# Performance work log

Measured on AMD Instinct MI355X. Metric: run time of the kernel, lower is better.

The kernel has to match this reference:

```python
import jax, jax.numpy as jnp
import numpy as np

HIDDEN = 1024
N_HEAD = 16
HEAD_DIM = HIDDEN // N_HEAD

def setup_inputs() -> dict:
    key = jax.random.key(0)
    ks = jax.random.split(key, 5)
    B, T = 2, 2048
    s_in = 1.0 / np.sqrt(HIDDEN)
    return {
        "x": jax.random.normal(ks[0], (B, T, HIDDEN), dtype=jnp.float32),
        "w_attn": jax.random.normal(ks[1], (HIDDEN, 3 * HIDDEN), dtype=jnp.float32) * s_in,
        "b_attn": jnp.zeros((3 * HIDDEN,), dtype=jnp.float32),
        "w_proj": jax.random.normal(ks[2], (HIDDEN, HIDDEN), dtype=jnp.float32) * s_in,
        "b_proj": jnp.zeros((HIDDEN,), dtype=jnp.float32),
    }

def reference(x, w_attn, b_attn, w_proj, b_proj):
    B, T, C = x.shape
    qkv = x @ w_attn + b_attn  # (B, T, 3C)
    q, k, v = jnp.split(qkv, 3, axis=-1)
    # (B, H, T, D)
    q = q.reshape(B, T, N_HEAD, HEAD_DIM).transpose(0, 2, 1, 3)
    k = k.reshape(B, T, N_HEAD, HEAD_DIM).transpose(0, 2, 1, 3)
    v = v.reshape(B, T, N_HEAD, HEAD_DIM).transpose(0, 2, 1, 3)
    scale = 1.0 / np.sqrt(HEAD_DIM).astype(np.float32)
    attn = jnp.einsum('bhqd,bhkd->bhqk', q, k) * scale
    causal = jnp.tril(jnp.ones((T, T), dtype=bool))
    attn = jnp.where(causal[None, None], attn, -jnp.inf)
    attn = jax.nn.softmax(attn, axis=-1)
    out = jnp.einsum('bhqk,bhkd->bhqd', attn, v)
    out = out.transpose(0, 2, 1, 3).reshape(B, T, C)
    return out @ w_proj + b_proj
```

## Files before the change

### kernel.cpp

```cpp
#include <hip/hip_runtime.h>
#include <stdint.h>

#define T_SEQ 2048
#define NB 2
#define NH 16
#define HD 64
#define HID 1024
#define MTOK (NB * T_SEQ)

typedef float f32x4 __attribute__((ext_vector_type(4)));
typedef float f32x16 __attribute__((ext_vector_type(16)));
typedef short bf16x8 __attribute__((ext_vector_type(8)));
typedef unsigned short u16;
typedef unsigned int u32;

#define QSCALE 0.1803368801f

__device__ __forceinline__ u16 f2bf(float f) {
  union { float f; uint32_t u; } v; v.f = f;
  return (u16)((v.u + 0x7fffu + ((v.u >> 16) & 1u)) >> 16);
}

__device__ __forceinline__ void gl_lds16(const void* g, void* l) {
  __builtin_amdgcn_global_load_lds(
      (const __attribute__((address_space(1))) unsigned int*)g,
      (__attribute__((address_space(3))) unsigned int*)l, 16, 0, 0);
}

__global__ void convert_k(const float* __restrict__ in, u16* __restrict__ out, int n4) {
  int i = blockIdx.x * blockDim.x + threadIdx.x;
  int stride = gridDim.x * blockDim.x;
  for (; i < n4; i += stride) {
    float4 f = ((const float4*)in)[i];
    ushort4 o;
    o.x = f2bf(f.x); o.y = f2bf(f.y); o.z = f2bf(f.z); o.w = f2bf(f.w);
    ((ushort4*)out)[i] = o;
  }
}

__global__ void transpose_k(const float* __restrict__ in, u16* __restrict__ out, int R, int C) {
  __shared__ float tile[32][33];
  int c0 = blockIdx.x * 32, r0 = blockIdx.y * 32;
  int tx = threadIdx.x, ty = threadIdx.y;
#pragma unroll
  for (int i = 0; i < 32; i += 8)
    tile[ty + i][tx] = in[(size_t)(r0 + ty + i) * C + c0 + tx];
  __syncthreads();
#pragma unroll
  for (int i = 0; i < 32; i += 8)
    out[(size_t)(c0 + ty + i) * R + r0 + tx] = f2bf(tile[tx][ty + i]);
}

template <int MODE>
__global__ __launch_bounds__(256, 4)
void gemm_k(const u16* __restrict__ A, const u16* __restrict__ Bt,
            const float* __restrict__ bias,
            u16* __restrict__ q, u16* __restrict__ kk, u16* __restrict__ v,
            float* __restrict__ outf) {
  __shared__ __align__(16) char lds[32768];
  const int tid = threadIdx.x, wid = tid >> 6, lane = tid & 63;
  const int m0 = blockIdx.y * 128, n0 = blockIdx.x * 128;
  const int wm = (wid >> 1) * 64, wn = (wid & 1) * 64;

  f32x4 acc[4][4];
  const f32x4 z = {0.f, 0.f, 0.f, 0.f};
#pragma unroll
  for (int mi = 0; mi < 4; ++mi)
#pragma unroll
    for (int ni = 0; ni < 4; ++ni) acc[mi][ni] = z;

  const int srow = tid >> 2;
  const int scb = (tid & 3) << 4;
  const int scsrc = (scb ^ ((srow & 3) << 4)) >> 1;
  const int rA = lane & 15;
  const int kbyte = (lane >> 4) << 4;

#define GSTAGE(tt_)                                                              \
  do {                                                                           \
    const int k0_ = (tt_) << 5;                                                  \
    char* ab_ = lds + (((tt_) & 1) << 13);                                       \
    char* bb_ = lds + 16384 + (((tt_) & 1) << 13);                               \
    gl_lds16(A + (size_t)(m0 + srow) * HID + k0_ + scsrc, ab_ + wid * 1024);     \
    gl_lds16(A + (size_t)(m0 + 64 + srow) * HID + k0_ + scsrc, ab_ + 4096 + wid * 1024); \
    gl_lds16(Bt + (size_t)(n0 + srow) * HID + k0_ + scsrc, bb_ + wid * 1024);    \
    gl_lds16(Bt + (size_t)(n0 + 64 + srow) * HID + k0_ + scsrc, bb_ + 4096 + wid * 1024); \
  } while (0)

  GSTAGE(0);
  GSTAGE(1);

  for (int tt = 0; tt < 32; ++tt) {
    if (tt < 31)
      asm volatile("s_waitcnt vmcnt(4)" ::: "memory");
    else
      asm volatile("s_waitcnt vmcnt(0)" ::: "memory");
    __builtin_amdgcn_s_barrier();
    __builtin_amdgcn_sched_barrier(0);

    const char* ab = lds + ((tt & 1) << 13);
    const char* bb = lds + 16384 + ((tt & 1) << 13);
    bf16x8 a[4], b[4];
#pragma unroll
    for (int mi = 0; mi < 4; ++mi) {
      const int row = wm + mi * 16 + rA;
      a[mi] = *(const bf16x8*)(ab + row * 64 + (kbyte ^ ((row & 3) << 4)));
    }
#pragma unroll
    for (int ni = 0; ni < 4; ++ni) {
      const int row = wn + ni * 16 + rA;
      b[ni] = *(const bf16x8*)(bb + row * 64 + (kbyte ^ ((row & 3) << 4)));
    }
#pragma unroll
    for (int mi = 0; mi < 4; ++mi)
#pragma unroll
      for (int ni = 0; ni < 4; ++ni)
        acc[mi][ni] = __builtin_amdgcn_mfma_f32_16x16x32_bf16(a[mi], b[ni], acc[mi][ni], 0, 0, 0);

    __builtin_amdgcn_s_barrier();
    __builtin_amdgcn_sched_barrier(0);
    if (tt < 30) GSTAGE(tt + 2);
  }
#undef GSTAGE

  const int coll = lane & 15, rowl = (lane >> 4) << 2;
#pragma unroll
  for (int mi = 0; mi < 4; ++mi) {
#pragma unroll
    for (int ni = 0; ni < 4; ++ni) {
      const int n = n0 + wn + ni * 16 + coll;
      const float bv = bias[n];
#pragma unroll
      for (int r = 0; r < 4; ++r) {
        const int m = m0 + wm + mi * 16 + rowl + r;
        float val = acc[mi][ni][r] + bv;
        if (MODE == 0) {
          const int reg = n >> 10, c = n & 1023, h = c >> 6, d = c & 63;
          const int bb2 = m >> 11, t = m & 2047;
          if (reg == 0) q[((size_t)(bb2 * NH + h) * T_SEQ + t) * HD + d] = f2bf(val * QSCALE);
          else if (reg == 1) kk[((size_t)(bb2 * NH + h) * T_SEQ + t) * HD + d] = f2bf(val);
          else v[((size_t)(bb2 * NH + h) * HD + d) * T_SEQ + t] = f2bf(val);
        } else {
          outf[(size_t)m * HID + n] = val;
        }
      }
    }
  }
}

__global__ __launch_bounds__(512, 4)
void attn_k(const u16* __restrict__ Q, const u16* __restrict__ K,
            const u16* __restrict__ Vt, u16* __restrict__ AO) {
  __shared__ __align__(16) char lds[65536];
  const int tid = threadIdx.x;
  const int lane = tid & 63;
  const int wid = tid >> 6;
  const int qsub = wid & 3, par = wid >> 2;
  const int bid = blockIdx.x;
  const int halfg = bid >> 8, r8 = bid & 255;
  const int bh = (r8 & 7) * 4 + ((r8 >> 3) & 3);
  const int lvl = r8 >> 5;
  const int qb = halfg ? lvl : (15 - lvl);
  const int q0 = qb * 128;
  const int ql = lane & 31, h = lane >> 5;
  const bool hi = (h != 0);

  const u16* Qg = Q + (size_t)bh * T_SEQ * HD;
  const u16* Kg = K + (size_t)bh * T_SEQ * HD;
  const u16* Vg = Vt + (size_t)bh * T_SEQ * HD;

  const int q0w = q0 + qsub * 32;
  const int dq = 2 * qb + (qsub >> 1);

  bf16x8 qf[4];
#pragma unroll
  for (int s = 0; s < 4; ++s)
    qf[s] = *(const bf16x8*)(Qg + (size_t)(q0w + ql) * HD + s * 16 + h * 8);

  f32x16 ot0, ot1;
#pragma unroll
  for (int i = 0; i < 16; ++i) { ot0[i] = 0.f; ot1[i] = 0.f; }
  float m = -3.0e38f, l = 0.f;

  const int srow = tid >> 3;
  const int scb = (tid & 7) << 4;
  const int sc0 = (scb ^ ((srow & 7) << 4)) >> 1;

  const int nsup = qb + 1;

#define STAGE(tt_)                                                            \
  do {                                                                        \
    const int kv0_ = (tt_) << 6;                                              \
    gl_lds16(Kg + (size_t)(kv0_ + srow) * HD + sc0,                           \
             lds + (((tt_) & 3) << 13) + wid * 1024);                         \
    gl_lds16(Vg + (size_t)srow * T_SEQ + kv0_ + sc0,                          \
             lds + 32768 + (((tt_) & 3) << 13) + wid * 1024);                 \
  } while (0)

  STAGE(0);
  STAGE(1);

  for (int ss = 0; ss < nsup; ++ss) {
    if (ss + 1 < nsup) {
      STAGE(2 * ss + 2);
      STAGE(2 * ss + 3);
      asm volatile("s_waitcnt vmcnt(4)" ::: "memory");
    } else {
      asm volatile("s_waitcnt vmcnt(0)" ::: "memory");
    }
    __builtin_amdgcn_s_barrier();
    __builtin_amdgcn_sched_barrier(0);

    const int tt = 2 * ss + par;
    if (tt <= dq) {
      const int kv0 = tt << 6;
      const char* kb = lds + ((tt & 3) << 13);
      const char* vb = lds + 32768 + ((tt & 3) << 13);
      f32x16 s0, s1;
#pragma unroll
      for (int i = 0; i < 16; ++i) { s0[i] = 0.f; s1[i] = 0.f; }
#pragma unroll
      for (int s = 0; s < 4; ++s) {
        const int cb = 32 * s + 16 * h;
        const int r0 = ql, r1 = 32 + ql;
        bf16x8 kf0 = *(const bf16x8*)(kb + r0 * 128 + (cb ^ ((r0 & 7) << 4)));
        bf16x8 kf1 = *(const bf16x8*)(kb + r1 * 128 + (cb ^ ((r1 & 7) << 4)));
        s0 = __builtin_amdgcn_mfma_f32_32x32x16_bf16(kf0, qf[s], s0, 0, 0, 0);
        s1 = __builtin_amdgcn_mfma_f32_32x32x16_bf16(kf1, qf[s], s1, 0, 0, 0);
      }
      if (tt == dq) {
        const int qg = q0w + ql;
#pragma unroll
        for (int r = 0; r < 16; ++r) {
          const int kvl = (r & 3) + 8 * (r >> 2) + 4 * h;
          if (kv0 + kvl > qg) s0[r] = -3.0e38f;
          if (kv0 + 32 + kvl > qg) s1[r] = -3.0e38f;
        }
      }
      float mx[16];
#pragma unroll
      for (int i = 0; i < 16; ++i) mx[i] = fmaxf(s0[i], s1[i]);
#pragma unroll
      for (int d = 8; d; d >>= 1)
#pragma unroll
        for (int i = 0; i < d; ++i) mx[i] = fmaxf(mx[i], mx[i + d]);
      const float tm = fmaxf(mx[0], __shfl_xor(mx[0], 32, 64));
      if (!__all(tm <= m + 4.0f)) {
        const float mnew = fmaxf(m, tm);
        const float fold = __builtin_amdgcn_exp2f(m - mnew);
        m = mnew;
        l *= fold;
#pragma unroll
        for (int i = 0; i < 16; ++i) { ot0[i] *= fold; ot1[i] *= fold; }
      }
#pragma unroll
      for (int i = 0; i < 16; ++i) {
        s0[i] = __builtin_amdgcn_exp2f(s0[i] - m);
        s1[i] = __builtin_amdgcn_exp2f(s1[i] - m);
      }
      float sm[16];
#pragma unroll
      for (int i = 0; i < 16; ++i) sm[i] = s0[i] + s1[i];
#pragma unroll
      for (int d = 8; d; d >>= 1)
#pragma unroll
        for (int i = 0; i < d; ++i) sm[i] += sm[i + d];
      l += sm[0] + __shfl_xor(sm[0], 32, 64);

      u32 w0[8], w1[8];
#pragma unroll
      for (int mm = 0; mm < 8; ++mm) {
        asm("v_cvt_pk_bf16_f32 %0, %1, %2" : "=v"(w0[mm]) : "v"(s0[2 * mm]), "v"(s0[2 * mm + 1]));
        asm("v_cvt_pk_bf16_f32 %0, %1, %2" : "=v"(w1[mm]) : "v"(s1[2 * mm]), "v"(s1[2 * mm + 1]));
      }
#pragma unroll
      for (int sb = 0; sb < 2; ++sb) {
#pragma unroll
        for (int t = 0; t < 2; ++t) {
          u32 a0 = sb ? w1[4 * t]     : w0[4 * t];
          u32 a1 = sb ? w1[4 * t + 1] : w0[4 * t + 1];
          u32 a2 = sb ? w1[4 * t + 2] : w0[4 * t + 2];
          u32 a3 = sb ? w1[4 * t + 3] : w0[4 * t + 3];
          u32 snd0 = hi ? a0 : a2;
          u32 snd1 = hi ? a1 : a3;
          u32 own0 = hi ? a2 : a0;
          u32 own1 = hi ? a3 : a1;
          u32 p0 = __shfl_xor(snd0, 32, 64);
          u32 p1 = __shfl_xor(snd1, 32, 64);
          union { u32 u[4]; bf16x8 v; } fr;
          fr.u[0] = hi ? p0 : own0;
          fr.u[1] = hi ? p1 : own1;
          fr.u[2] = hi ? own0 : p0;
          fr.u[3] = hi ? own1 : p1;
          const int s = sb * 2 + t;
          const int cb = 32 * s + 16 * h;
          const int r0 = ql, r1 = 32 + ql;
          bf16x8 vf0 = *(const bf16x8*)(vb + r0 * 128 + (cb ^ ((r0 & 7) << 4)));
          bf16x8 vf1 = *(const bf16x8*)(vb + r1 * 128 + (cb ^ ((r1 & 7) << 4)));
          ot0 = __builtin_amdgcn_mfma_f32_32x32x16_bf16(vf0, fr.v, ot0, 0, 0, 0);
          ot1 = __builtin_amdgcn_mfma_f32_32x32x16_bf16(vf1, fr.v, ot1, 0, 0, 0);
        }
      }
    }
    __builtin_amdgcn_s_barrier();
    __builtin_amdgcn_sched_barrier(0);
  }
#undef STAGE

  float* R = (float*)(lds + qsub * 8448);
  if (par == 1) {
#pragma unroll
    for (int r = 0; r < 16; ++r) {
      const int dl = (r & 3) + 8 * (r >> 2) + 4 * h;
      R[ql * 66 + dl] = ot0[r];
      R[ql * 66 + 32 + dl] = ot1[r];
    }
    if (!hi) { R[ql * 66 + 64] = m; R[ql * 66 + 65] = l; }
  }
  __builtin_amdgcn_s_barrier();
  if (par == 1) return;

  const float m2 = R[ql * 66 + 64];
  const float l2 = R[ql * 66 + 65];
  const float M = fmaxf(m, m2);
  const float c1 = __builtin_amdgcn_exp2f(m - M);
  const float c2 = __builtin_amdgcn_exp2f(m2 - M);
  const float L = c1 * l + c2 * l2;
  const float inv = 1.0f / L;
  float of0[16], of1[16];
#pragma unroll
  for (int r = 0; r < 16; ++r) {
    const int dl = (r & 3) + 8 * (r >> 2) + 4 * h;
    of0[r] = (c1 * ot0[r] + c2 * R[ql * 66 + dl]) * inv;
    of1[r] = (c1 * ot1[r] + c2 * R[ql * 66 + 32 + dl]) * inv;
  }
  asm volatile("s_waitcnt lgkmcnt(0)" ::: "memory");
  __builtin_amdgcn_sched_barrier(0);

  float* E = (float*)(lds + qsub * 8448);
#pragma unroll
  for (int r = 0; r < 16; ++r) {
    const int dl = (r & 3) + 8 * (r >> 2) + 4 * h;
    E[dl * 33 + ql] = of0[r];
    E[(dl + 32) * 33 + ql] = of1[r];
  }
  asm volatile("s_waitcnt lgkmcnt(0)" ::: "memory");
  __builtin_amdgcn_sched_barrier(0);
  const int bb = bh >> 4, hh = bh & 15;
  const int r2 = lane >> 3;
  const int c8 = (lane & 7) * 8;
#pragma unroll
  for (int g = 0; g < 4; ++g) {
    const int qrow = g * 8 + r2;
    union { u16 a[8]; bf16x8 v; } ov;
#pragma unroll
    for (int j = 0; j < 8; ++j) ov.a[j] = f2bf(E[(c8 + j) * 33 + qrow]);
    *(bf16x8*)(AO + (size_t)(bb * T_SEQ + q0 + qsub * 32 + qrow) * HID + hh * HD + c8) = ov.v;
  }
}

extern "C" void kernel_launch(void* const* d_in, const int* in_sizes, int n_in,
                              void* d_out, int out_size, void* d_ws, size_t ws_size,
                              hipStream_t stream) {
  const float* x      = (const float*)d_in[0];
  const float* w_attn = (const float*)d_in[1];
  const float* b_attn = (const float*)d_in[2];
  const float* w_proj = (const float*)d_in[3];
  const float* b_proj = (const float*)d_in[4];
  float* out = (float*)d_out;

  char* ws = (char*)d_ws;
  u16* xb   = (u16*)(ws);
  u16* wabT = (u16*)(ws + (size_t)(8  << 20));
  u16* wpbT = (u16*)(ws + (size_t)(14 << 20));
  u16* q    = (u16*)(ws + (size_t)(16 << 20));
  u16* k    = (u16*)(ws + (size_t)(24 << 20));
  u16* v    = (u16*)(ws + (size_t)(32 << 20));
  u16* ao   = (u16*)(ws + (size_t)(40 << 20));

  convert_k<<<dim3(1024), dim3(256), 0, stream>>>(x, xb, MTOK * HID / 4);
  transpose_k<<<dim3(96, 32), dim3(32, 8), 0, stream>>>(w_attn, wabT, HID, 3 * HID);
  transpose_k<<<dim3(32, 32), dim3(32, 8), 0, stream>>>(w_proj, wpbT, HID, HID);
  gemm_k<0><<<dim3(24, 32), dim3(256), 0, stream>>>(xb, wabT, b_attn, q, k, v, nullptr);
  attn_k<<<dim3(512), dim3(512), 0, stream>>>(q, k, v, ao);
  gemm_k<1><<<dim3(8, 32), dim3(256), 0, stream>>>(ao, wpbT, b_proj, nullptr, nullptr, nullptr, out);
}
```

Baseline: 108.5 us.

## Triple-buffer GEMM loads and use 256-row tiles for QKV projection

```diff
diff --git a/kernel.cpp b/kernel.cpp
--- a/kernel.cpp
+++ b/kernel.cpp
@@ -51,15 +51,17 @@
     out[(size_t)(c0 + ty + i) * R + r0 + tx] = f2bf(tile[tx][ty + i]);
 }
 
-template <int MODE>
-__global__ __launch_bounds__(256, 4)
+template <int MODE, int BM>
+__global__ __launch_bounds__((BM == 256) ? 512 : 256, (BM == 256) ? 4 : 3)
 void gemm_k(const u16* __restrict__ A, const u16* __restrict__ Bt,
             const float* __restrict__ bias,
             u16* __restrict__ q, u16* __restrict__ kk, u16* __restrict__ v,
             float* __restrict__ outf) {
-  __shared__ __align__(16) char lds[32768];
+  constexpr int ABUF = BM * 64;
+  constexpr int BBUF = 8192;
+  __shared__ __align__(16) char lds[3 * (ABUF + BBUF)];
   const int tid = threadIdx.x, wid = tid >> 6, lane = tid & 63;
-  const int m0 = blockIdx.y * 128, n0 = blockIdx.x * 128;
+  const int m0 = blockIdx.y * BM, n0 = blockIdx.x * 128;
   const int wm = (wid >> 1) * 64, wn = (wid & 1) * 64;
 
   f32x4 acc[4][4];
@@ -75,30 +77,43 @@
   const int rA = lane & 15;
   const int kbyte = (lane >> 4) << 4;
 
-#define GSTAGE(tt_)                                                              \
-  do {                                                                           \
-    const int k0_ = (tt_) << 5;                                                  \
-    char* ab_ = lds + (((tt_) & 1) << 13);                                       \
-    char* bb_ = lds + 16384 + (((tt_) & 1) << 13);                               \
-    gl_lds16(A + (size_t)(m0 + srow) * HID + k0_ + scsrc, ab_ + wid * 1024);     \
-    gl_lds16(A + (size_t)(m0 + 64 + srow) * HID + k0_ + scsrc, ab_ + 4096 + wid * 1024); \
-    gl_lds16(Bt + (size_t)(n0 + srow) * HID + k0_ + scsrc, bb_ + wid * 1024);    \
-    gl_lds16(Bt + (size_t)(n0 + 64 + srow) * HID + k0_ + scsrc, bb_ + 4096 + wid * 1024); \
+#define GSTAGE(tt_, bi_)                                                             \
+  do {                                                                               \
+    const int k0_ = (tt_) << 5;                                                      \
+    char* ab_ = lds + (bi_) * ABUF;                                                  \
+    char* bb_ = lds + 3 * ABUF + (bi_) * BBUF;                                       \
+    if constexpr (BM == 256) {                                                       \
+      gl_lds16(A + (size_t)(m0 + srow) * HID + k0_ + scsrc, ab_ + wid * 1024);       \
+      gl_lds16(A + (size_t)(m0 + 128 + srow) * HID + k0_ + scsrc, ab_ + 8192 + wid * 1024); \
+      gl_lds16(Bt + (size_t)(n0 + srow) * HID + k0_ + scsrc, bb_ + wid * 1024);      \
+    } else {                                                                         \
+      gl_lds16(A + (size_t)(m0 + srow) * HID + k0_ + scsrc, ab_ + wid * 1024);       \
+      gl_lds16(A + (size_t)(m0 + 64 + srow) * HID + k0_ + scsrc, ab_ + 4096 + wid * 1024); \
+      gl_lds16(Bt + (size_t)(n0 + srow) * HID + k0_ + scsrc, bb_ + wid * 1024);      \
+      gl_lds16(Bt + (size_t)(n0 + 64 + srow) * HID + k0_ + scsrc, bb_ + 4096 + wid * 1024); \
+    }                                                                                \
   } while (0)
 
-  GSTAGE(0);
-  GSTAGE(1);
-
+  GSTAGE(0, 0);
+  GSTAGE(1, 1);
+  GSTAGE(2, 2);
+
+  int cur = 0;
   for (int tt = 0; tt < 32; ++tt) {
-    if (tt < 31)
-      asm volatile("s_waitcnt vmcnt(4)" ::: "memory");
-    else
-      asm volatile("s_waitcnt vmcnt(0)" ::: "memory");
+    if constexpr (BM == 256) {
+      if (tt < 30)       asm volatile("s_waitcnt vmcnt(6)" ::: "memory");
+      else if (tt == 30) asm volatile("s_waitcnt vmcnt(3)" ::: "memory");
+      else               asm volatile("s_waitcnt vmcnt(0)" ::: "memory");
+    } else {
+      if (tt < 30)       asm volatile("s_waitcnt vmcnt(8)" ::: "memory");
+      else if (tt == 30) asm volatile("s_waitcnt vmcnt(4)" ::: "memory");
+      else               asm volatile("s_waitcnt vmcnt(0)" ::: "memory");
+    }
     __builtin_amdgcn_s_barrier();
     __builtin_amdgcn_sched_barrier(0);
 
-    const char* ab = lds + ((tt & 1) << 13);
-    const char* bb = lds + 16384 + ((tt & 1) << 13);
+    const char* ab = lds + cur * ABUF;
+    const char* bb = lds + 3 * ABUF + cur * BBUF;
     bf16x8 a[4], b[4];
 #pragma unroll
     for (int mi = 0; mi < 4; ++mi) {
@@ -118,7 +133,8 @@
 
     __builtin_amdgcn_s_barrier();
     __builtin_amdgcn_sched_barrier(0);
-    if (tt < 30) GSTAGE(tt + 2);
+    if (tt + 3 < 32) GSTAGE(tt + 3, cur);
+    cur = (cur == 2) ? 0 : cur + 1;
   }
 #undef GSTAGE
 
@@ -380,7 +396,7 @@
   convert_k<<<dim3(1024), dim3(256), 0, stream>>>(x, xb, MTOK * HID / 4);
   transpose_k<<<dim3(96, 32), dim3(32, 8), 0, stream>>>(w_attn, wabT, HID, 3 * HID);
   transpose_k<<<dim3(32, 32), dim3(32, 8), 0, stream>>>(w_proj, wpbT, HID, HID);
-  gemm_k<0><<<dim3(24, 32), dim3(256), 0, stream>>>(xb, wabT, b_attn, q, k, v, nullptr);
+  gemm_k<0, 256><<<dim3(24, 16), dim3(512), 0, stream>>>(xb, wabT, b_attn, q, k, v, nullptr);
   attn_k<<<dim3(512), dim3(512), 0, stream>>>(q, k, v, ao);
-  gemm_k<1><<<dim3(8, 32), dim3(256), 0, stream>>>(ao, wpbT, b_proj, nullptr, nullptr, nullptr, out);
-}
+  gemm_k<1, 128><<<dim3(8, 32), dim3(256), 0, stream>>>(ao, wpbT, b_proj, nullptr, nullptr, nullptr, out);
+}
```

Result: slower. 115.3 us (+6.2%).
